# Kernel tuning notes

Measured on AMD Instinct MI355X. Metric: run time of the kernel, lower is better.

Reference implementation:

```python
import jax, jax.numpy as jnp
import numpy as np

B, D, H = 4096, 32, 1024  # batch, in_out_dim, hidden width


def setup_inputs() -> dict:
    key = jax.random.key(0)
    ks = jax.random.split(key, 10)

    def lin_w(k, shape, fan_in):
        bound = 1.0 / np.sqrt(fan_in)
        return jax.random.uniform(k, shape, jnp.float32, -bound, bound)

    return {
        "t": jax.random.uniform(ks[0], (1,), jnp.float32),
        "z": jax.random.normal(ks[1], (B, D), jnp.float32),
        "W0": lin_w(ks[2], (H, D + 1), D + 1),
        "b0": lin_w(ks[3], (H,), D + 1),
        "W1": lin_w(ks[4], (H, H), H),
        "b1": lin_w(ks[5], (H,), H),
        "W2": lin_w(ks[6], (H, H), H),
        "b2": lin_w(ks[7], (H,), H),
        "W3": lin_w(ks[8], (D, H), H),
        "b3": lin_w(ks[9], (D,), H),
    }


def _mlp(v, params):
    # Linear -> Tanh chain, final Linear (torch convention y = x @ W.T + b)
    for W, b in params[:-1]:
        v = jnp.tanh(v @ W.T + b)
    W, b = params[-1]
    return v @ W.T + b


def reference(t, z, W0, b0, W1, b1, W2, b2, W3, b3):
    bsz, d = z.shape
    tt = jnp.broadcast_to(t.reshape(-1), (bsz,))  # check_t: repeat scalar t
    params = [(W0, b0), (W1, b1), (W2, b2), (W3, b3)]

    def f(zz):  # [B, D] -> [B, D]
        v = jnp.concatenate([zz, tt[:, None]], axis=1)  # [B, D+1]
        return _mlp(v, params)

    out = f(z)

    # Exact Jacobian trace via d forward-mode JVPs (replaces the per-dim
    # autograd.grad loop in trace_df_dz with a single vmapped JVP batch).
    eye = jnp.eye(d, dtype=z.dtype)

    def jvp_i(e):
        return jax.jvp(f, (z,), (jnp.broadcast_to(e, z.shape),))[1]  # [B, D]

    tang = jax.vmap(jvp_i)(eye)            # [D, B, D]
    trace = jnp.einsum("ibi->b", tang)     # sum_i df_i/dz_i per sample
    divv = -trace
    return out, divv[:, None]
```

## Files before the change

kernel.cpp:

```cpp
#include <hip/hip_runtime.h>
#include <hip/hip_bf16.h>
#include <stdint.h>


using bf  = __hip_bfloat16;
using bf2 = __hip_bfloat162;
typedef __attribute__((ext_vector_type(8))) short bf16x8;
typedef __attribute__((ext_vector_type(4))) float f32x4;

__device__ __forceinline__ float b2f(bf x)    { return __bfloat162float(x); }
__device__ __forceinline__ bf    f2b(float x) { return __float2bfloat16(x); }

__device__ __forceinline__ void gld16(const void* g, void* l) {
  __builtin_amdgcn_global_load_lds((const __attribute__((address_space(1))) void*)g,
                                   (__attribute__((address_space(3))) void*)l,
                                   16, 0, 0);
}

__device__ __forceinline__ void conv_body(int blk, const float* __restrict__ src,
                                          bf* __restrict__ dst, int n4) {
  const int i = blk * 256 + threadIdx.x;
  if (i >= n4) return;
  float4 v = ((const float4*)src)[i];
  bf2* d = (bf2*)(dst + (size_t)i * 4);
  d[0] = __float22bfloat162_rn(make_float2(v.x, v.y));
  d[1] = __float22bfloat162_rn(make_float2(v.z, v.w));
}

__device__ __forceinline__ void w0t_body(int blk, const float* __restrict__ W0,
                                         bf* __restrict__ W0T) {
  const int idx = blk * 256 + threadIdx.x;
  const int i = idx >> 10, q = idx & 1023;
  W0T[idx] = f2b(W0[q * 33 + i]);
}

__global__ __launch_bounds__(256) void prep_k(const float* __restrict__ z,
                                              const float* __restrict__ tin,
                                              const float* __restrict__ W0,
                                              const float* __restrict__ b0,
                                              const float* __restrict__ W1,
                                              const float* __restrict__ W2,
                                              const float* __restrict__ W3,
                                              bf* __restrict__ h0,
                                              bf* __restrict__ W0T,
                                              bf* __restrict__ W1b,
                                              bf* __restrict__ W2b,
                                              bf* __restrict__ W3b,
                                              float* __restrict__ out2) {
  __shared__ float zs[32 * 33];
  const int f = blockIdx.x, t = threadIdx.x;
  if (f < 128) {
    const int s0 = f * 32;
    for (int j = t; j < 1024; j += 256) {
      const int s = j >> 5, k = j & 31;
      zs[s * 33 + k] = z[(size_t)(s0 + s) * 32 + k];
    }
    if (t < 32) zs[t * 33 + 32] = tin[0];
    __syncthreads();
#pragma unroll 1
    for (int rep = 0; rep < 4; ++rep) {
      const int hh = rep * 256 + t;
      const float* wr = W0 + (size_t)hh * 33;
      float wv[33];
#pragma unroll
      for (int k = 0; k < 33; ++k) wv[k] = wr[k];
      const float bv = b0[hh];
#pragma unroll 1
      for (int s = 0; s < 32; ++s) {
        float acc = bv;
#pragma unroll
        for (int k = 0; k < 33; ++k) acc += wv[k] * zs[s * 33 + k];
        h0[(size_t)(s0 + s) * 1024 + hh] = f2b(tanhf(acc));
      }
    }
  } else if (f < 1152) {
    conv_body(f - 128, W1, W1b, 262144);
  } else if (f < 2176) {
    conv_body(f - 1152, W2, W2b, 262144);
  } else if (f < 2208) {
    conv_body(f - 2176, W3, W3b, 8192);
  } else if (f < 2336) {
    w0t_body(f - 2208, W0, W0T);
  } else {
#pragma unroll
    for (int u = 0; u < 16; ++u) out2[u * 256 + t] = 0.f;
  }
}

__device__ __forceinline__ void gemm_core(bf* As, bf* Bs,
                                          const bf* __restrict__ A,
                                          const bf* __restrict__ B,
                                          size_t m0, size_t n0,
                                          f32x4 (&acc)[8][4]) {
  constexpr int K = 1024;
  const int t = threadIdx.x, l = t & 63, w = t >> 6;
  const int wm = w >> 1, wn = w & 1;
  const int r15 = l & 15, q4 = l >> 4, sw = r15 & 7;

  const int lrow = l >> 3;
  const int lseg = (l & 7) ^ lrow;
  const bf* asrc[8]; bf* alds[8];
  const bf* bsrc[4]; bf* blds[4];
#pragma unroll
  for (int u = 0; u < 8; ++u) {
    const int row = w * 64 + u * 8 + lrow;
    asrc[u] = A + (m0 + row) * K + lseg * 8;
    alds[u] = As + (size_t)(w * 64 + u * 8) * 64;
  }
#pragma unroll
  for (int u = 0; u < 4; ++u) {
    const int row = w * 32 + u * 8 + lrow;
    bsrc[u] = B + (n0 + row) * K + lseg * 8;
    blds[u] = Bs + (size_t)(w * 32 + u * 8) * 64;
  }

#pragma unroll 1
  for (int k0 = 0; k0 < K; k0 += 64) {
#pragma unroll
    for (int u = 0; u < 8; ++u) gld16(asrc[u] + k0, alds[u]);
#pragma unroll
    for (int u = 0; u < 4; ++u) gld16(bsrc[u] + k0, blds[u]);
    __syncthreads();
#pragma unroll
    for (int kk = 0; kk < 2; ++kk) {
      const int sa = (kk * 4 + q4) ^ sw;
      bf16x8 af[8], bfr[4];
#pragma unroll
      for (int i = 0; i < 8; ++i)
        af[i] = *(const bf16x8*)(As + (wm * 128 + i * 16 + r15) * 64 + sa * 8);
#pragma unroll
      for (int j = 0; j < 4; ++j)
        bfr[j] = *(const bf16x8*)(Bs + (wn * 64 + j * 16 + r15) * 64 + sa * 8);
#pragma unroll
      for (int mi = 0; mi < 8; ++mi)
#pragma unroll
        for (int ni = 0; ni < 4; ++ni)
          acc[mi][ni] = __builtin_amdgcn_mfma_f32_16x16x32_bf16(af[mi], bfr[ni], acc[mi][ni], 0, 0, 0);
    }
    __syncthreads();
  }
}

__global__ __launch_bounds__(256, 2) void gemm_fwd(const bf* __restrict__ A,
                                                   const bf* __restrict__ W,
                                                   const float* __restrict__ bias,
                                                   bf* __restrict__ H) {
  constexpr int N = 1024;
  __shared__ __align__(16) bf As[256 * 64];
  __shared__ __align__(16) bf Bs[128 * 64];
  const int t = threadIdx.x, l = t & 63, w = t >> 6;
  const int wm = w >> 1, wn = w & 1;
  const int f = blockIdx.x;
  const int n_t = (f >> 3) & 7, m_t = (f & 7) + 8 * (f >> 6);
  const size_t m0 = (size_t)m_t * 256, n0 = (size_t)n_t * 128;
  const int r15 = l & 15, q4 = l >> 4;
  f32x4 acc[8][4] = {};
  gemm_core(As, Bs, A, W, m0, n0, acc);
#pragma unroll
  for (int ni = 0; ni < 4; ++ni) {
    const int n = (int)n0 + wn * 64 + ni * 16 + r15;
    const float bv = bias[n];
#pragma unroll
    for (int mi = 0; mi < 8; ++mi)
#pragma unroll
      for (int r = 0; r < 4; ++r) {
        const size_t m = m0 + wm * 128 + mi * 16 + q4 * 4 + r;
        H[m * N + n] = f2b(tanhf(acc[mi][ni][r] + bv));
      }
  }
}

__global__ __launch_bounds__(256) void fwd3_k(const bf* __restrict__ h2,
                                              const bf* __restrict__ W3b,
                                              const float* __restrict__ b3,
                                              float* __restrict__ out) {
  __shared__ __align__(16) bf hs[8 * 1024];
  const int t = threadIdx.x;
  const size_t bb = (size_t)blockIdx.x * 8;
  const uint4* src = (const uint4*)(h2 + bb * 1024);
  uint4* dv = (uint4*)hs;
#pragma unroll
  for (int j = 0; j < 4; ++j) dv[j * 256 + t] = src[j * 256 + t];
  __syncthreads();
  const int i = t & 31, bl = t >> 5;
  const bf2* hr = (const bf2*)(hs + bl * 1024);
  const bf2* wr = (const bf2*)(W3b + (size_t)i * 1024);
  float s = 0.f;
#pragma unroll 8
  for (int k2 = 0; k2 < 512; ++k2) {
    float2 a = __bfloat1622float2(hr[k2]);
    float2 c = __bfloat1622float2(wr[k2]);
    s += a.x * c.x + a.y * c.y;
  }
  out[(bb + bl) * 32 + i] = s + b3[i];
}

__global__ __launch_bounds__(256) void t0_k(const bf* __restrict__ h0c,
                                            const bf* __restrict__ W0T,
                                            bf* __restrict__ T0) {
  const int idx = blockIdx.x * 256 + threadIdx.x;
  const int m = idx >> 6, seg = idx & 63;
  const int b = m >> 5, i = m & 31;
  const bf2* hp = (const bf2*)(h0c + (size_t)b * 1024 + seg * 16);
  const bf2* wp = (const bf2*)(W0T + (size_t)i * 1024 + seg * 16);
  bf2* dp = (bf2*)(T0 + (size_t)m * 1024 + seg * 16);
#pragma unroll
  for (int u = 0; u < 8; ++u) {
    float2 h = __bfloat1622float2(hp[u]);
    float2 w = __bfloat1622float2(wp[u]);
    float2 r;
    r.x = (1.f - h.x * h.x) * w.x;
    r.y = (1.f - h.y * h.y) * w.y;
    dp[u] = __float22bfloat162_rn(r);
  }
}

__global__ __launch_bounds__(256, 2) void gemm_jvp1(const bf* __restrict__ T0,
                                                    const bf* __restrict__ W1b,
                                                    const bf* __restrict__ h1c,
                                                    bf* __restrict__ T1) {
  constexpr int N = 1024;
  __shared__ __align__(16) bf As[256 * 64];
  __shared__ __align__(16) bf Bs[128 * 64];
  const int t = threadIdx.x, l = t & 63, w = t >> 6;
  const int wm = w >> 1, wn = w & 1;
  const int f = blockIdx.x;
  const int n_t = (f >> 3) & 7, m_t = (f & 7) + 8 * (f >> 6);
  const size_t m0 = (size_t)m_t * 256, n0 = (size_t)n_t * 128;
  const int r15 = l & 15, q4 = l >> 4;
  f32x4 acc[8][4] = {};
  gemm_core(As, Bs, T0, W1b, m0, n0, acc);
  const int bbase = (int)((m0 + wm * 128) >> 5);
#pragma unroll
  for (int ni = 0; ni < 4; ++ni) {
    const int n = (int)n0 + wn * 64 + ni * 16 + r15;
    float a1v[4];
#pragma unroll
    for (int s = 0; s < 4; ++s) {
      const float hv = b2f(h1c[(size_t)(bbase + s) * 1024 + n]);
      a1v[s] = 1.f - hv * hv;
    }
#pragma unroll
    for (int mi = 0; mi < 8; ++mi)
#pragma unroll
      for (int r = 0; r < 4; ++r) {
        const size_t m = m0 + wm * 128 + mi * 16 + q4 * 4 + r;
        T1[m * N + n] = f2b(a1v[mi >> 1] * acc[mi][ni][r]);
      }
  }
}

__global__ __launch_bounds__(256, 2) void gemm_jvp2(const bf* __restrict__ T1,
                                                    const bf* __restrict__ W2b,
                                                    const bf* __restrict__ W3b,
                                                    const bf* __restrict__ h2c,
                                                    float* __restrict__ out2c) {
  __shared__ __align__(16) bf As[256 * 64];
  __shared__ __align__(16) bf Bs[128 * 64];
  const int t = threadIdx.x, l = t & 63, w = t >> 6;
  const int wm = w >> 1, wn = w & 1;
  const int f = blockIdx.x;
  const int n_t = (f >> 3) & 7, m_t = (f & 7) + 8 * (f >> 6);
  const size_t m0 = (size_t)m_t * 256, n0 = (size_t)n_t * 128;
  const int r15 = l & 15, q4 = l >> 4;
  f32x4 acc[8][4] = {};
  gemm_core(As, Bs, T1, W2b, m0, n0, acc);
  const int bbase = (int)((m0 + wm * 128) >> 5);
  float part[4] = {0.f, 0.f, 0.f, 0.f};
#pragma unroll
  for (int ni = 0; ni < 4; ++ni) {
    const int n = (int)n0 + wn * 64 + ni * 16 + r15;
    float a2v[4];
#pragma unroll
    for (int s = 0; s < 4; ++s) {
      const float hv = b2f(h2c[(size_t)(bbase + s) * 1024 + n]);
      a2v[s] = 1.f - hv * hv;
    }
#pragma unroll
    for (int mi = 0; mi < 8; ++mi) {
      const int isel = mi >> 1;
#pragma unroll
      for (int r = 0; r < 4; ++r) {
        const int mm = wm * 128 + mi * 16 + q4 * 4 + r;
        part[isel] += b2f(W3b[(size_t)(mm & 31) * 1024 + n]) * a2v[isel] * acc[mi][ni][r];
      }
    }
  }
#pragma unroll
  for (int off = 32; off > 0; off >>= 1) {
#pragma unroll
    for (int s = 0; s < 4; ++s) part[s] += __shfl_down(part[s], off);
  }
  if (l == 0) {
#pragma unroll
    for (int s = 0; s < 4; ++s) atomicAdd(out2c + bbase + s, -part[s]);
  }
}

extern "C" void kernel_launch(void* const* d_in, const int* in_sizes, int n_in,
                              void* d_out, int out_size, void* d_ws, size_t ws_size,
                              hipStream_t stream) {
  const float* tin = (const float*)d_in[0];
  const float* z   = (const float*)d_in[1];
  const float* W0  = (const float*)d_in[2];
  const float* b0  = (const float*)d_in[3];
  const float* W1  = (const float*)d_in[4];
  const float* b1  = (const float*)d_in[5];
  const float* W2  = (const float*)d_in[6];
  const float* b2  = (const float*)d_in[7];
  const float* W3  = (const float*)d_in[8];
  const float* b3  = (const float*)d_in[9];
  float* out = (float*)d_out;
  float* out2 = out + 131072;
  (void)in_sizes; (void)n_in; (void)out_size;

  char* ws = (char*)d_ws;
  size_t off = 0;
  auto take = [&](size_t bytes) {
    char* p = ws + off;
    off = (off + bytes + 255) & ~(size_t)255;
    return p;
  };
  bf* h0   = (bf*)take((size_t)4096 * 1024 * 2);
  bf* h1   = (bf*)take((size_t)4096 * 1024 * 2);
  bf* h2   = (bf*)take((size_t)4096 * 1024 * 2);
  bf* W0T  = (bf*)take((size_t)32 * 1024 * 2);
  bf* W1b  = (bf*)take((size_t)1024 * 1024 * 2);
  bf* W2b  = (bf*)take((size_t)1024 * 1024 * 2);
  bf* W3b  = (bf*)take((size_t)32 * 1024 * 2);
  const size_t avail = (ws_size > off) ? (ws_size - off) : 0;
  int NB = 4096;
  while (NB > 256 && 2 * (size_t)NB * 65536 > avail) NB >>= 1;
  bf* T0 = (bf*)take((size_t)NB * 65536);
  bf* T1 = (bf*)take((size_t)NB * 65536);

  prep_k<<<dim3(2337), dim3(256), 0, stream>>>(z, tin, W0, b0, W1, W2, W3,
                                               h0, W0T, W1b, W2b, W3b, out2);
  gemm_fwd<<<dim3(128), dim3(256), 0, stream>>>(h0, W1b, b1, h1);
  gemm_fwd<<<dim3(128), dim3(256), 0, stream>>>(h1, W2b, b2, h2);
  fwd3_k<<<dim3(512), dim3(256), 0, stream>>>(h2, W3b, b3, out);
  for (int cb = 0; cb < 4096; cb += NB) {
    t0_k<<<dim3(NB * 8), dim3(256), 0, stream>>>(h0 + (size_t)cb * 1024, W0T, T0);
    gemm_jvp1<<<dim3(NB), dim3(256), 0, stream>>>(
        T0, W1b, h1 + (size_t)cb * 1024, T1);
    gemm_jvp2<<<dim3(NB), dim3(256), 0, stream>>>(
        T1, W2b, W3b, h2 + (size_t)cb * 1024, out2 + cb);
  }
}
```

Measured before the change: 817.9 us.

## Use 256x256 tiles with 8-wave double-buffered pipelined GEMM for JVP passes

Replaces the 256x128, 4-wave JVP GEMMs with 512-thread blocks computing 256x256 tiles. The new core double-buffers A and B in 128KB of LDS using direct global-to-LDS loads, XOR-swizzled layouts, and interleaved wave-priority MFMA phases. The goal is to halve B re-reads per output and overlap global loads with MFMA work. The cost is much higher LDS use per block, which limits occupancy, and hand-written waitcnt and barrier sequencing that could be fragile.

```diff
diff --git a/kernel.cpp b/kernel.cpp
--- a/kernel.cpp
+++ b/kernel.cpp
@@ -215,21 +215,104 @@
   }
 }
 
-__global__ __launch_bounds__(256, 2) void gemm_jvp1(const bf* __restrict__ T0,
-                                                    const bf* __restrict__ W1b,
-                                                    const bf* __restrict__ h1c,
-                                                    bf* __restrict__ T1) {
-  constexpr int N = 1024;
-  __shared__ __align__(16) bf As[256 * 64];
-  __shared__ __align__(16) bf Bs[128 * 64];
+__device__ __forceinline__ void gemm8_core(bf* lds,
+                                           const bf* __restrict__ A,
+                                           const bf* __restrict__ B,
+                                           size_t m0, size_t n0,
+                                           f32x4 (&acc)[8][4]) {
+  constexpr int K = 1024;
   const int t = threadIdx.x, l = t & 63, w = t >> 6;
-  const int wm = w >> 1, wn = w & 1;
+  const int wm = w >> 2, wn = w & 3;
+  const int r15 = l & 15, q4 = l >> 4;
+  const int lrow = l >> 3, lseg = (l & 7) ^ lrow;
+  const int w8 = w * 8;
+
+  bf* As0 = lds;          bf* As1 = lds + 16384;
+  bf* Bs0 = lds + 32768;  bf* Bs1 = lds + 49152;
+
+  const bf* Ag = A + (m0 + (size_t)(w8 + lrow)) * K + lseg * 8;
+  const bf* Bg = B + (n0 + (size_t)(w8 + lrow)) * K + lseg * 8;
+
+  const int sa0 = q4 ^ (r15 & 7);
+  const int aoff = (wm * 128 + r15) * 64;
+  const int boff = (wn * 64 + r15) * 64;
+
+  bf16x8 bfr[4][2];
+  bf16x8 af[2][2];
+
+  auto ldB = [&](const bf* Bsp) {
+#pragma unroll
+    for (int ni = 0; ni < 4; ++ni) {
+      bfr[ni][0] = *(const bf16x8*)(Bsp + boff + ni * 1024 + sa0 * 8);
+      bfr[ni][1] = *(const bf16x8*)(Bsp + boff + ni * 1024 + (sa0 ^ 4) * 8);
+    }
+  };
+  auto ldA = [&](const bf* Asp, int q) {
+#pragma unroll
+    for (int s = 0; s < 2; ++s) {
+      af[s][0] = *(const bf16x8*)(Asp + aoff + (2 * q + s) * 1024 + sa0 * 8);
+      af[s][1] = *(const bf16x8*)(Asp + aoff + (2 * q + s) * 1024 + (sa0 ^ 4) * 8);
+    }
+  };
+  auto stA = [&](bf* dst, int kt, int h) {
+    gld16(Ag + (size_t)(h * 128) * K + kt * 64,      dst + (h * 128 + w8) * 64);
+    gld16(Ag + (size_t)(h * 128 + 64) * K + kt * 64, dst + (h * 128 + 64 + w8) * 64);
+  };
+  auto stB = [&](bf* dst, int kt, int h) {
+    gld16(Bg + (size_t)(h * 128) * K + kt * 64,      dst + (h * 128 + w8) * 64);
+    gld16(Bg + (size_t)(h * 128 + 64) * K + kt * 64, dst + (h * 128 + 64 + w8) * 64);
+  };
+  auto mmq = [&](int q) {
+    __builtin_amdgcn_s_barrier();
+    asm volatile("s_waitcnt lgkmcnt(0)");
+    __builtin_amdgcn_s_setprio(1);
+#pragma unroll
+    for (int kk = 0; kk < 2; ++kk)
+#pragma unroll
+      for (int s = 0; s < 2; ++s)
+#pragma unroll
+        for (int ni = 0; ni < 4; ++ni)
+          acc[2 * q + s][ni] = __builtin_amdgcn_mfma_f32_16x16x32_bf16(
+              af[s][kk], bfr[ni][kk], acc[2 * q + s][ni], 0, 0, 0);
+    __builtin_amdgcn_s_setprio(0);
+    __builtin_amdgcn_s_barrier();
+  };
+
+  stA(As0, 0, 0); stA(As0, 0, 1);
+  stB(Bs0, 0, 0); stB(Bs0, 0, 1);
+  stB(Bs1, 1, 0); stB(Bs1, 1, 1);
+  asm volatile("s_waitcnt vmcnt(4)" ::: "memory");
+  __builtin_amdgcn_s_barrier();
+
+#pragma unroll 1
+  for (int j = 0; j < 8; ++j) {
+    const int o = 2 * j + 1, e2 = (2 * j + 2) & 15, o2 = (2 * j + 3) & 15;
+    ldB(Bs0); ldA(As0, 0); stA(As1, o, 0);            mmq(0);
+    ldA(As0, 1);           stA(As1, o, 1);            mmq(1);
+    ldA(As0, 2);           stB(Bs0, e2, 0);           mmq(2);
+    ldA(As0, 3);           stB(Bs0, e2, 1);
+    asm volatile("s_waitcnt vmcnt(4)" ::: "memory");  mmq(3);
+    ldB(Bs1); ldA(As1, 0); stA(As0, e2, 0);           mmq(0);
+    ldA(As1, 1);           stA(As0, e2, 1);           mmq(1);
+    ldA(As1, 2);           stB(Bs1, o2, 0);           mmq(2);
+    ldA(As1, 3);           stB(Bs1, o2, 1);
+    asm volatile("s_waitcnt vmcnt(4)" ::: "memory");  mmq(3);
+  }
+  asm volatile("s_waitcnt vmcnt(0)" ::: "memory");
+}
+
+__global__ __launch_bounds__(512, 2) void gemm8_jvp1(const bf* __restrict__ T0,
+                                                     const bf* __restrict__ W1b,
+                                                     const bf* __restrict__ h1c,
+                                                     bf* __restrict__ T1) {
+  __shared__ __align__(16) bf lds[65536];
   const int f = blockIdx.x;
-  const int n_t = (f >> 3) & 7, m_t = (f & 7) + 8 * (f >> 6);
-  const size_t m0 = (size_t)m_t * 256, n0 = (size_t)n_t * 128;
+  const size_t m0 = (size_t)(f >> 2) * 256, n0 = (size_t)(f & 3) * 256;
+  f32x4 acc[8][4] = {};
+  gemm8_core(lds, T0, W1b, m0, n0, acc);
+  const int t = threadIdx.x, l = t & 63, w = t >> 6;
+  const int wm = w >> 2, wn = w & 3;
   const int r15 = l & 15, q4 = l >> 4;
-  f32x4 acc[8][4] = {};
-  gemm_core(As, Bs, T0, W1b, m0, n0, acc);
   const int bbase = (int)((m0 + wm * 128) >> 5);
 #pragma unroll
   for (int ni = 0; ni < 4; ++ni) {
@@ -245,26 +328,24 @@
 #pragma unroll
       for (int r = 0; r < 4; ++r) {
         const size_t m = m0 + wm * 128 + mi * 16 + q4 * 4 + r;
-        T1[m * N + n] = f2b(a1v[mi >> 1] * acc[mi][ni][r]);
+        T1[m * 1024 + n] = f2b(a1v[mi >> 1] * acc[mi][ni][r]);
       }
   }
 }
 
-__global__ __launch_bounds__(256, 2) void gemm_jvp2(const bf* __restrict__ T1,
-                                                    const bf* __restrict__ W2b,
-                                                    const bf* __restrict__ W3b,
-                                                    const bf* __restrict__ h2c,
-                                                    float* __restrict__ out2c) {
-  __shared__ __align__(16) bf As[256 * 64];
-  __shared__ __align__(16) bf Bs[128 * 64];
+__global__ __launch_bounds__(512, 2) void gemm8_jvp2(const bf* __restrict__ T1,
+                                                     const bf* __restrict__ W2b,
+                                                     const bf* __restrict__ W3b,
+                                                     const bf* __restrict__ h2c,
+                                                     float* __restrict__ out2c) {
+  __shared__ __align__(16) bf lds[65536];
+  const int f = blockIdx.x;
+  const size_t m0 = (size_t)(f >> 2) * 256, n0 = (size_t)(f & 3) * 256;
+  f32x4 acc[8][4] = {};
+  gemm8_core(lds, T1, W2b, m0, n0, acc);
   const int t = threadIdx.x, l = t & 63, w = t >> 6;
-  const int wm = w >> 1, wn = w & 1;
-  const int f = blockIdx.x;
-  const int n_t = (f >> 3) & 7, m_t = (f & 7) + 8 * (f >> 6);
-  const size_t m0 = (size_t)m_t * 256, n0 = (size_t)n_t * 128;
+  const int wm = w >> 2, wn = w & 3;
   const int r15 = l & 15, q4 = l >> 4;
-  f32x4 acc[8][4] = {};
-  gemm_core(As, Bs, T1, W2b, m0, n0, acc);
   const int bbase = (int)((m0 + wm * 128) >> 5);
   float part[4] = {0.f, 0.f, 0.f, 0.f};
 #pragma unroll
@@ -341,9 +422,9 @@
   fwd3_k<<<dim3(512), dim3(256), 0, stream>>>(h2, W3b, b3, out);
   for (int cb = 0; cb < 4096; cb += NB) {
     t0_k<<<dim3(NB * 8), dim3(256), 0, stream>>>(h0 + (size_t)cb * 1024, W0T, T0);
-    gemm_jvp1<<<dim3(NB), dim3(256), 0, stream>>>(
+    gemm8_jvp1<<<dim3(NB / 2), dim3(512), 0, stream>>>(
         T0, W1b, h1 + (size_t)cb * 1024, T1);
-    gemm_jvp2<<<dim3(NB), dim3(256), 0, stream>>>(
+    gemm8_jvp2<<<dim3(NB / 2), dim3(512), 0, stream>>>(
         T1, W2b, W3b, h2 + (size_t)cb * 1024, out2 + cb);
   }
 }
```

After: 824.2 us. About the same (+0.8%).
